# Kernel tuning notes

Hardware: AMD Instinct MI355X
Metric: run time of the kernel (lower is better)

Reference implementation:

```python
import jax, jax.numpy as jnp
import numpy as np

N, LQ, C = 1, 12240, 256
HEADS, LEVELS, FRAMES, POINTS = 8, 4, 4, 4
D_HEAD = C // HEADS  # 32
SHAPES = np.array([[48, 48, 4], [24, 24, 4], [12, 12, 4], [6, 6, 4]], np.int32)  # (H, W, T)
LEN_IN = int((SHAPES[:, 0] * SHAPES[:, 1] * SHAPES[:, 2]).sum())  # 12240
assert LEN_IN == LQ


def setup_inputs() -> dict:
    key = jax.random.key(0)
    ks = jax.random.split(key, 9)
    starts = np.concatenate([[0], np.cumsum(SHAPES[:, 0] * SHAPES[:, 1] * SHAPES[:, 2])[:-1]]).astype(np.int32)
    off_dim = HEADS * LEVELS * FRAMES * POINTS * 2
    attn_dim = HEADS * LEVELS * FRAMES * POINTS
    s = 1.0 / np.sqrt(C)
    return {
        "query": jax.random.normal(ks[0], (N, LQ, C), jnp.float32),
        "reference_points": jax.random.uniform(ks[1], (N, LQ, LEVELS, 2), dtype=jnp.float32),
        "temporal_offsets": 0.05 * jax.random.normal(ks[2], (LQ, LEVELS, FRAMES, 2), jnp.float32),
        "input_flatten": jax.random.normal(ks[3], (N, LEN_IN, C), jnp.float32),
        "input_spatial_shapes": jnp.asarray(SHAPES),
        "input_level_start_index": jnp.asarray(starts),
        "W_off": 0.01 * jax.random.normal(ks[4], (C, off_dim), jnp.float32),
        "b_off": 0.1 * jax.random.normal(ks[5], (off_dim,), jnp.float32),
        "W_attn": 0.02 * jax.random.normal(ks[6], (C, attn_dim), jnp.float32),
        "b_attn": jnp.zeros((attn_dim,), jnp.float32),
        "W_val": s * jax.random.normal(ks[7], (C, C), jnp.float32),
        "b_val": jnp.zeros((C,), jnp.float32),
        "W_out": s * jax.random.normal(ks[8], (C, C), jnp.float32),
        "b_out": jnp.zeros((C,), jnp.float32),
    }


def ms_deform_core(value, shapes_hw, starts, loc, attn_w):
    """value: (N, Len_in, Hh, D); loc: (N, Lq, Hh, L, P, 2) in [0,1];
    attn_w: (N, Lq, Hh, L, P); shapes_hw/starts: python ints per level.
    Bilinear sampling matches F.grid_sample(align_corners=False, padding_mode='zeros')."""
    n, _, hh, d = value.shape
    lq, p = loc.shape[1], loc.shape[4]
    out = jnp.zeros((n, hh, lq, d), value.dtype)
    for lid, (hl, wl) in enumerate(shapes_hw):
        s0 = starts[lid]
        v = jnp.transpose(value[:, s0:s0 + hl * wl], (0, 2, 1, 3))  # (N, Hh, H*W, D)
        x = loc[:, :, :, lid, :, 0] * wl - 0.5  # (N, Lq, Hh, P) pixel coords
        y = loc[:, :, :, lid, :, 1] * hl - 0.5
        x0 = jnp.floor(x)
        y0 = jnp.floor(y)
        fx, fy = x - x0, y - y0
        x0i, y0i = x0.astype(jnp.int32), y0.astype(jnp.int32)
        acc = jnp.zeros((n, hh, lq, p, d), value.dtype)
        corners = ((0, 0, (1 - fx) * (1 - fy)), (0, 1, fx * (1 - fy)),
                   (1, 0, (1 - fx) * fy), (1, 1, fx * fy))
        for dy, dx, w in corners:
            xi, yi = x0i + dx, y0i + dy
            valid = (xi >= 0) & (xi < wl) & (yi >= 0) & (yi < hl)
            idx = jnp.clip(yi, 0, hl - 1) * wl + jnp.clip(xi, 0, wl - 1)  # (N, Lq, Hh, P)
            idx_t = jnp.transpose(idx, (0, 2, 1, 3)).reshape(n, hh, lq * p, 1)
            g = jnp.take_along_axis(v, idx_t, axis=2).reshape(n, hh, lq, p, d)
            wm = jnp.transpose(jnp.where(valid, w, 0.0), (0, 2, 1, 3))  # (N, Hh, Lq, P)
            acc = acc + g * wm[..., None]
        aw = jnp.transpose(attn_w[:, :, :, lid], (0, 2, 1, 3))  # (N, Hh, Lq, P)
        out = out + jnp.sum(acc * aw[..., None], axis=3)
    return jnp.transpose(out, (0, 2, 1, 3)).reshape(n, lq, hh * d)


def reference(query, reference_points, temporal_offsets, input_flatten,
              input_spatial_shapes, input_level_start_index,
              W_off, b_off, W_attn, b_attn, W_val, b_val, W_out, b_out):
    shapes = np.asarray(input_spatial_shapes)  # static (L, 3) = (H, W, T)
    starts = [int(s) for s in np.asarray(input_level_start_index)]
    n, lq, _ = query.shape
    value = (input_flatten @ W_val + b_val).reshape(n, -1, HEADS, D_HEAD)
    attn = jax.nn.softmax((query @ W_attn + b_attn)
                          .reshape(n, lq, HEADS, LEVELS * FRAMES * POINTS), axis=-1)
    attn = attn.reshape(n, lq, HEADS, LEVELS, FRAMES * POINTS)
    off = (query @ W_off + b_off).reshape(n, lq, HEADS, LEVELS, FRAMES, POINTS, 2)
    # offset_normalizer = (T, H*W) per level: x spans frames, y spans flattened pixels
    norm = jnp.stack([jnp.asarray(shapes[:, 2], jnp.float32),
                      jnp.asarray(shapes[:, 0] * shapes[:, 1], jnp.float32)], axis=-1)  # (L, 2)
    loc = temporal_offsets[None, :, None, :, :, None, :] + off / norm[None, None, None, :, None, None, :]
    loc = loc.reshape(n, lq, HEADS, LEVELS, FRAMES * POINTS, 2)
    loc = reference_points[:, :, None, :, None, :] + loc
    shapes_hw = [(int(h) * int(w), int(t)) for h, w, t in shapes]  # (H*W, T) grids
    out = ms_deform_core(value, shapes_hw, starts, loc, attn)
    return out @ W_out + b_out
```

## Files before the change

### kernel.cpp

```cpp
#include <hip/hip_runtime.h>
#include <hip/hip_bf16.h>
#include <hip/hip_fp16.h>

#define LQ     12240

typedef _Float16 half8 __attribute__((ext_vector_type(8)));
typedef float floatx4 __attribute__((ext_vector_type(4)));
typedef unsigned int uint;

__global__ __launch_bounds__(256) void prep_all(
    const float* __restrict__ query, const float* __restrict__ inflat,
    const float* __restrict__ W_val, const float* __restrict__ W_attn,
    const float* __restrict__ W_off, const float* __restrict__ W_out,
    __half* __restrict__ qh, __half* __restrict__ ifh,
    __half* __restrict__ wT_val, __half* __restrict__ wT_ao,
    __half* __restrict__ wT_out, int n4each) {
  int b = blockIdx.x;
  if (b < 512) {
    const float* in;
    __half* out;
    int N;
    if (b < 64) { in = W_val; out = wT_val; N = 256; }
    else if (b < 192) { b -= 64; in = W_attn; out = wT_ao; N = 512; }
    else if (b < 448) { b -= 192; in = W_off; out = wT_ao + (size_t)512 * 256; N = 1024; }
    else { b -= 448; in = W_out; out = wT_out; N = 256; }
    const int nb = N / 32;
    const int n0 = (b % nb) * 32, k0 = (b / nb) * 32;

    __shared__ float t[32][33];
    const int c = threadIdx.x & 31, r = threadIdx.x >> 5;
#pragma unroll
    for (int i = 0; i < 4; ++i)
      t[r + i * 8][c] = in[(size_t)(k0 + r + i * 8) * N + n0 + c];
    __syncthreads();
#pragma unroll
    for (int i = 0; i < 4; ++i)
      out[(size_t)(n0 + r + i * 8) * 256 + k0 + c] = __float2half(t[c][r + i * 8]);
    return;
  }
  int i = (b - 512) * 256 + threadIdx.x;
  const float* in = query;
  __half* out = qh;
  if (i >= n4each) { in = inflat; out = ifh; i -= n4each; }
  const float4 v = reinterpret_cast<const float4*>(in)[i];
  const __half2 p0 = __floats2half2_rn(v.x, v.y);
  const __half2 p1 = __floats2half2_rn(v.z, v.w);
  uint2 pk;
  pk.x = *reinterpret_cast<const uint*>(&p0);
  pk.y = *reinterpret_cast<const uint*>(&p1);
  reinterpret_cast<uint2*>(out)[i] = pk;
}

__global__ __launch_bounds__(256) void gemm_all(
    const __half* __restrict__ qh, const __half* __restrict__ ifh,
    const __half* __restrict__ wT_val, const __half* __restrict__ wT_ao,
    const float* __restrict__ b_val, const float* __restrict__ b_attn,
    const float* __restrict__ b_off,
    __half* __restrict__ val_t, __half* __restrict__ ao_h, int M) {
  __shared__ uint4 As_g[128 * 8];
  __shared__ uint4 Bs_g[128 * 8];

  const int tid = threadIdx.x;

  const int nwg = gridDim.x * gridDim.y;
  int bid = blockIdx.y * gridDim.x + blockIdx.x;
  bid = (bid & 7) * (nwg >> 3) + (bid >> 3);
  const int bx = bid % gridDim.x;
  const int bm = (bid / gridDim.x) * 128;

  const bool isval = (bx < 2);
  const int bn = isval ? bx * 128 : (bx - 2) * 128;
  const __half* __restrict__ A  = isval ? ifh : qh;
  const __half* __restrict__ Bt = isval ? wT_val : wT_ao;
  const float* __restrict__ bias = isval ? b_val : (bn < 512 ? b_attn : b_off);
  const int coff = (!isval && bn >= 512) ? 512 : 0;

  const int wid = tid >> 6, lane = tid & 63;
  const int wr = wid >> 1, wn = wid & 1;
  const int l16 = lane & 15, lhi = lane >> 4;

  floatx4 acc[4][4] = {};

  const int srow = tid >> 1;
  const int sg0 = (tid & 1) * 4;
  const bool arow_ok = (bm + srow) < M;
  const __half* Arow = A + (size_t)(arow_ok ? bm + srow : 0) * 256;
  const __half* Brow = Bt + (size_t)(bn + srow) * 256;

  for (int ks = 0; ks < 4; ++ks) {
    const int k0 = ks * 64;
#pragma unroll
    for (int i = 0; i < 4; ++i) {
      const int g = sg0 + i;
      uint4 av = make_uint4(0, 0, 0, 0);
      if (arow_ok) av = *reinterpret_cast<const uint4*>(Arow + k0 + g * 8);
      As_g[srow * 8 + (g ^ (srow & 7))] = av;
      Bs_g[srow * 8 + (g ^ (srow & 7))] =
          *reinterpret_cast<const uint4*>(Brow + k0 + g * 8);
    }
    __syncthreads();

#pragma unroll
    for (int kk = 0; kk < 2; ++kk) {
      half8 a[4], b[4];
#pragma unroll
      for (int m = 0; m < 4; ++m) {
        const int row = wr * 64 + m * 16 + l16;
        const int g = kk * 4 + lhi;
        union { uint4 u; half8 h; } cv;
        cv.u = As_g[row * 8 + (g ^ (row & 7))];
        a[m] = cv.h;
      }
#pragma unroll
      for (int n = 0; n < 4; ++n) {
        const int row = wn * 64 + n * 16 + l16;
        const int g = kk * 4 + lhi;
        union { uint4 u; half8 h; } cv;
        cv.u = Bs_g[row * 8 + (g ^ (row & 7))];
        b[n] = cv.h;
      }
#pragma unroll
      for (int m = 0; m < 4; ++m)
#pragma unroll
        for (int n = 0; n < 4; ++n)
          acc[m][n] = __builtin_amdgcn_mfma_f32_16x16x32_f16(a[m], b[n], acc[m][n], 0, 0, 0);
    }
    __syncthreads();
  }

#pragma unroll
  for (int m = 0; m < 4; ++m) {
    const int row0 = bm + wr * 64 + m * 16 + lhi * 4;
#pragma unroll
    for (int n = 0; n < 4; ++n) {
      const int col = bn + wn * 64 + n * 16 + l16;
      const float bv = bias[col - coff];
#pragma unroll
      for (int r = 0; r < 4; ++r) {
        const int row = row0 + r;
        if (row < M) {
          const float v = acc[m][n][r] + bv;
          if (isval) {
            val_t[(size_t)(col >> 5) * ((size_t)M * 32) + (size_t)row * 32 + (col & 31)] = __float2half(v);
          } else {
            ao_h[(size_t)row * 1536 + col] = __float2half(v);
          }
        }
      }
    }
  }
}

__global__ __launch_bounds__(256) void gemm_out(
    const __half* __restrict__ A, const __half* __restrict__ Bt,
    const float* __restrict__ bias, float* __restrict__ C, int M, int N) {
  __shared__ uint4 As_g[128 * 8];
  __shared__ uint4 Bs_g[128 * 8];

  const int tid = threadIdx.x;
  const int nwg = gridDim.x * gridDim.y;
  int bid = blockIdx.y * gridDim.x + blockIdx.x;
  bid = (bid & 7) * (nwg >> 3) + (bid >> 3);
  const int bm = (bid / gridDim.x) * 128, bn = (bid % gridDim.x) * 128;

  const int wid = tid >> 6, lane = tid & 63;
  const int wr = wid >> 1, wn = wid & 1;
  const int l16 = lane & 15, lhi = lane >> 4;

  floatx4 acc[4][4] = {};

  const int srow = tid >> 1;
  const int sg0 = (tid & 1) * 4;
  const bool arow_ok = (bm + srow) < M;
  const __half* Arow = A + (size_t)(arow_ok ? bm + srow : 0) * 256;
  const __half* Brow = Bt + (size_t)(bn + srow) * 256;

  for (int ks = 0; ks < 4; ++ks) {
    const int k0 = ks * 64;
#pragma unroll
    for (int i = 0; i < 4; ++i) {
      const int g = sg0 + i;
      uint4 av = make_uint4(0, 0, 0, 0);
      if (arow_ok) av = *reinterpret_cast<const uint4*>(Arow + k0 + g * 8);
      As_g[srow * 8 + (g ^ (srow & 7))] = av;
      Bs_g[srow * 8 + (g ^ (srow & 7))] =
          *reinterpret_cast<const uint4*>(Brow + k0 + g * 8);
    }
    __syncthreads();

#pragma unroll
    for (int kk = 0; kk < 2; ++kk) {
      half8 a[4], b[4];
#pragma unroll
      for (int m = 0; m < 4; ++m) {
        const int row = wr * 64 + m * 16 + l16;
        const int g = kk * 4 + lhi;
        union { uint4 u; half8 h; } cv;
        cv.u = As_g[row * 8 + (g ^ (row & 7))];
        a[m] = cv.h;
      }
#pragma unroll
      for (int n = 0; n < 4; ++n) {
        const int row = wn * 64 + n * 16 + l16;
        const int g = kk * 4 + lhi;
        union { uint4 u; half8 h; } cv;
        cv.u = Bs_g[row * 8 + (g ^ (row & 7))];
        b[n] = cv.h;
      }
#pragma unroll
      for (int m = 0; m < 4; ++m)
#pragma unroll
        for (int n = 0; n < 4; ++n)
          acc[m][n] = __builtin_amdgcn_mfma_f32_16x16x32_f16(a[m], b[n], acc[m][n], 0, 0, 0);
    }
    __syncthreads();
  }

#pragma unroll
  for (int m = 0; m < 4; ++m) {
    const int row0 = bm + wr * 64 + m * 16 + lhi * 4;
#pragma unroll
    for (int n = 0; n < 4; ++n) {
      const int col = bn + wn * 64 + n * 16 + l16;
      const float bv = bias[col];
#pragma unroll
      for (int r = 0; r < 4; ++r) {
        const int row = row0 + r;
        if (row < M) C[(size_t)row * N + col] = acc[m][n][r] + bv;
      }
    }
  }
}

__device__ inline uint pack_wr(float w, uint row) {
  const __half hw = __float2half(w);
  return ((uint)__half_as_ushort(hw) << 16) | row;
}

__global__ __launch_bounds__(256, 8) void sample_kernel(
    const __half* __restrict__ value,
    const __half* __restrict__ ao,
    const float* __restrict__ tempoff,
    const float* __restrict__ refpts,
    __half* __restrict__ msout) {
  const int q0 = blockIdx.x * 2;
  const int tid = threadIdx.x;

  __shared__ __align__(16) uint spk[4096];
  float* slog = reinterpret_cast<float*>(spk);
  __shared__ float sm_m[16], sm_si[16];

#pragma unroll
  for (int k = 0; k < 4; ++k) {
    const int s = tid + k * 256;
    slog[s] = __half2float(ao[(size_t)(q0 + (s >> 9)) * 1536 + (s & 511)]);
  }
  __syncthreads();

  {
    const int g = tid >> 4;
    const int j = tid & 15;
    const float* e = &slog[g * 64];
    float m = fmaxf(fmaxf(e[j], e[j + 16]), fmaxf(e[j + 32], e[j + 48]));
#pragma unroll
    for (int mask = 8; mask >= 1; mask >>= 1) m = fmaxf(m, __shfl_xor(m, mask));
    float s = __expf(e[j] - m) + __expf(e[j + 16] - m) +
              __expf(e[j + 32] - m) + __expf(e[j + 48] - m);
#pragma unroll
    for (int mask = 8; mask >= 1; mask >>= 1) s += __shfl_xor(s, mask);
    if (j == 0) { sm_m[g] = m; sm_si[g] = 1.0f / s; }
  }
  __syncthreads();

  const float HWF[4] = {2304.f, 576.f, 144.f, 36.f};
  const float RHW[4] = {1.f / 2304.f, 1.f / 576.f, 1.f / 144.f, 1.f / 36.f};
  const int   S0[4]  = {0, 9216, 11520, 12096};
  const int   HWI[4] = {2304, 576, 144, 36};

  uint4 rec[4];
  int   ridx[4];
  const int h1   = tid & 7;
  const int smid = (tid >> 3) & 7;
  const int shi  = (tid >> 6) & 3;

#pragma unroll
  for (int k = 0; k < 4; ++k) {
    const int qi = k & 1;
    const int s  = smid | (shi << 3) | ((k >> 1) << 5);
    const int i  = h1 * 64 + s;
    const int l  = s >> 4;
    const int f  = (s >> 2) & 3;
    const size_t q = (size_t)(q0 + qi);
    const int g = (qi << 3) | h1;

    const float w = __expf(slog[(qi << 9) + i] - sm_m[g]) * sm_si[g];

    const float2 o  = __half22float2(*reinterpret_cast<const __half2*>(&ao[q * 1536 + 512 + i * 2]));
    const float2 to = *reinterpret_cast<const float2*>(&tempoff[q * 32 + (l * 4 + f) * 2]);
    const float2 rp = *reinterpret_cast<const float2*>(&refpts[q * 8 + l * 2]);

    const float hw = HWF[l];
    const float x = (to.x + o.x * 0.25f + rp.x) * 4.0f - 0.5f;
    const float y = (to.y + o.y * RHW[l] + rp.y) * hw - 0.5f;

    const float x0f = floorf(x), y0f = floorf(y);
    const float fx = x - x0f, fy = y - y0f;
    const int x0 = (int)x0f, y0 = (int)y0f;
    const int hl = HWI[l];

    const bool xv0 = (x0 >= 0) && (x0 < 4);
    const bool xv1 = (x0 >= -1) && (x0 < 3);
    const bool yv0 = (y0 >= 0) && (y0 < hl);
    const bool yv1 = (y0 >= -1) && (y0 < hl - 1);
    const int xc0 = min(max(x0, 0), 3);
    const int xc1 = min(max(x0 + 1, 0), 3);
    const int yc0 = min(max(y0, 0), hl - 1);
    const int yc1 = min(max(y0 + 1, 0), hl - 1);

    const float w00 = (xv0 && yv0) ? w * (1.f - fx) * (1.f - fy) : 0.f;
    const float w01 = (xv1 && yv0) ? w * fx * (1.f - fy) : 0.f;
    const float w10 = (xv0 && yv1) ? w * (1.f - fx) * fy : 0.f;
    const float w11 = (xv1 && yv1) ? w * fx * fy : 0.f;

    const int base = S0[l];
    rec[k] = make_uint4(pack_wr(w00, (uint)(base + yc0 * 4 + xc0)),
                        pack_wr(w01, (uint)(base + yc0 * 4 + xc1)),
                        pack_wr(w10, (uint)(base + yc1 * 4 + xc0)),
                        pack_wr(w11, (uint)(base + yc1 * 4 + xc1)));
    ridx[k] = (qi << 9) | (s << 3) | h1;
  }
  __syncthreads();

  uint4* spk4 = reinterpret_cast<uint4*>(spk);
#pragma unroll
  for (int k = 0; k < 4; ++k) spk4[ridx[k]] = rec[k];
  __syncthreads();

  const int qi = tid >> 7;
  const int h  = (tid >> 4) & 7;
  const int c  = (tid >> 2) & 3;
  const int d  = tid & 3;

  const uint* __restrict__ sp = spk + ((qi << 11) | (h << 2) | c);
  const char* __restrict__ vbase =
      (const char*)value + (size_t)h * LQ * 64 + d * 16;

  float f0 = 0.f, f1 = 0.f, f2 = 0.f, f3 = 0.f;
  float f4 = 0.f, f5 = 0.f, f6 = 0.f, f7 = 0.f;

#pragma unroll
  for (int l = 0; l < 4; ++l) {
    uint a0 = 0u, a1 = 0u, a2 = 0u, a3 = 0u;
#pragma unroll
    for (int t = 0; t < 16; ++t) {
      const uint pk = sp[(l * 16 + t) << 5];
      const uint4 v = *reinterpret_cast<const uint4*>(vbase + ((pk & 0xFFFFu) << 6));
      asm("v_pk_fma_f16 %0, %4, %5, %0 op_sel:[1,0,0]\n\t"
          "v_pk_fma_f16 %1, %4, %6, %1 op_sel:[1,0,0]\n\t"
          "v_pk_fma_f16 %2, %4, %7, %2 op_sel:[1,0,0]\n\t"
          "v_pk_fma_f16 %3, %4, %8, %3 op_sel:[1,0,0]"
          : "+v"(a0), "+v"(a1), "+v"(a2), "+v"(a3)
          : "v"(pk), "v"(v.x), "v"(v.y), "v"(v.z), "v"(v.w));
    }
    const float2 p0 = __half22float2(*reinterpret_cast<const __half2*>(&a0));
    const float2 p1 = __half22float2(*reinterpret_cast<const __half2*>(&a1));
    const float2 p2 = __half22float2(*reinterpret_cast<const __half2*>(&a2));
    const float2 p3 = __half22float2(*reinterpret_cast<const __half2*>(&a3));
    f0 += p0.x; f1 += p0.y; f2 += p1.x; f3 += p1.y;
    f4 += p2.x; f5 += p2.y; f6 += p3.x; f7 += p3.y;
  }

#pragma unroll
  for (int mask = 4; mask <= 8; mask <<= 1) {
    f0 += __shfl_xor(f0, mask); f1 += __shfl_xor(f1, mask);
    f2 += __shfl_xor(f2, mask); f3 += __shfl_xor(f3, mask);
    f4 += __shfl_xor(f4, mask); f5 += __shfl_xor(f5, mask);
    f6 += __shfl_xor(f6, mask); f7 += __shfl_xor(f7, mask);
  }

  if (c == 0) {
    const __half2 o0 = __floats2half2_rn(f0, f1);
    const __half2 o1 = __floats2half2_rn(f2, f3);
    const __half2 o2 = __floats2half2_rn(f4, f5);
    const __half2 o3 = __floats2half2_rn(f6, f7);
    uint4 st;
    st.x = *reinterpret_cast<const uint*>(&o0);
    st.y = *reinterpret_cast<const uint*>(&o1);
    st.z = *reinterpret_cast<const uint*>(&o2);
    st.w = *reinterpret_cast<const uint*>(&o3);
    *reinterpret_cast<uint4*>(&msout[(size_t)(q0 + qi) * 256 + h * 32 + d * 8]) = st;
  }
}

extern "C" void kernel_launch(void* const* d_in, const int* in_sizes, int n_in,
                              void* d_out, int out_size, void* d_ws, size_t ws_size,
                              hipStream_t stream) {
  const float* query   = (const float*)d_in[0];
  const float* refpts  = (const float*)d_in[1];
  const float* tempoff = (const float*)d_in[2];
  const float* inflat  = (const float*)d_in[3];
  const float* W_off  = (const float*)d_in[6];
  const float* b_off  = (const float*)d_in[7];
  const float* W_attn = (const float*)d_in[8];
  const float* b_attn = (const float*)d_in[9];
  const float* W_val  = (const float*)d_in[10];
  const float* b_val  = (const float*)d_in[11];
  const float* W_out  = (const float*)d_in[12];
  const float* b_out  = (const float*)d_in[13];

  char* ws = (char*)d_ws;
  const size_t szQ = (size_t)LQ * 256 * 2;
  __half* qh     = (__half*)ws;                 ws += szQ;
  __half* ifh    = (__half*)ws;                 ws += szQ;
  __half* wT_val = (__half*)ws;                 ws += (size_t)256 * 256 * 2;
  __half* wT_ao  = (__half*)ws;                 ws += (size_t)1536 * 256 * 2;
  __half* wT_out = (__half*)ws;                 ws += (size_t)256 * 256 * 2;
  __half* val_t  = (__half*)ws;                 ws += szQ;
  __half* ao_h   = (__half*)ws;                 ws += (size_t)LQ * 1536 * 2;
  __half* ms_h   = (__half*)ws;                 ws += szQ;

  const dim3 blk(256);
  const int n4each = LQ * 256 / 4;

  prep_all<<<dim3(512 + 2 * n4each / 256), blk, 0, stream>>>(
      query, inflat, W_val, W_attn, W_off, W_out,
      qh, ifh, wT_val, wT_ao, wT_out, n4each);

  const int gm = (LQ + 127) / 128;
  gemm_all<<<dim3(14, gm), blk, 0, stream>>>(qh, ifh, wT_val, wT_ao,
                                             b_val, b_attn, b_off,
                                             val_t, ao_h, LQ);

  sample_kernel<<<dim3(LQ / 2), blk, 0, stream>>>(val_t, ao_h, tempoff, refpts, ms_h);

  gemm_out<<<dim3(2, gm), blk, 0, stream>>>(ms_h, wT_out, b_out, (float*)d_out, LQ, 256);
}
```

Before: 124.8 us.

## Merge horizontally adjacent bilinear corners into one contiguous 128-byte gather per row

The bilinear corner records are restructured so each sample row (y0, y1) stores one base index plus a packed pair of half weights for the two adjacent x-corners. When the x-corners are not adjacent, for example after clamping at a border, both weights fold into the low slot. Threads now split 8 ways over a 128-byte span covering two neighbouring value rows, and pick the matching weight with a byte permute. This halves the number of shared-memory record reads and gather instructions per sample. In exchange it relies on the two x-corners being contiguous rows in the value layout and changes the reduction lane mapping.

```diff
diff --git a/kernel.cpp b/kernel.cpp
--- a/kernel.cpp
+++ b/kernel.cpp
@@ -232,9 +232,9 @@
   }
 }
 
-__device__ inline uint pack_wr(float w, uint row) {
-  const __half hw = __float2half(w);
-  return ((uint)__half_as_ushort(hw) << 16) | row;
+__device__ inline uint pack2h(float lo, float hi) {
+  const __half2 p = __floats2half2_rn(lo, hi);
+  return *reinterpret_cast<const uint*>(&p);
 }
 
 __global__ __launch_bounds__(256, 8) void sample_kernel(
@@ -317,16 +317,17 @@
     const int yc0 = min(max(y0, 0), hl - 1);
     const int yc1 = min(max(y0 + 1, 0), hl - 1);
 
-    const float w00 = (xv0 && yv0) ? w * (1.f - fx) * (1.f - fy) : 0.f;
-    const float w01 = (xv1 && yv0) ? w * fx * (1.f - fy) : 0.f;
-    const float w10 = (xv0 && yv1) ? w * (1.f - fx) * fy : 0.f;
-    const float w11 = (xv1 && yv1) ? w * fx * fy : 0.f;
+    const bool adj = (xc1 == xc0 + 1);
+    const float fxlo = (xv0 ? (1.f - fx) : 0.f) + ((!adj && xv1) ? fx : 0.f);
+    const float fxhi = (adj && xv1) ? fx : 0.f;
+    const float wy0 = yv0 ? w * (1.f - fy) : 0.f;
+    const float wy1 = yv1 ? w * fy : 0.f;
 
     const int base = S0[l];
-    rec[k] = make_uint4(pack_wr(w00, (uint)(base + yc0 * 4 + xc0)),
-                        pack_wr(w01, (uint)(base + yc0 * 4 + xc1)),
-                        pack_wr(w10, (uint)(base + yc1 * 4 + xc0)),
-                        pack_wr(w11, (uint)(base + yc1 * 4 + xc1)));
+    rec[k] = make_uint4((uint)(base + yc0 * 4 + xc0),
+                        pack2h(fxlo * wy0, fxhi * wy0),
+                        (uint)(base + yc1 * 4 + xc0),
+                        pack2h(fxlo * wy1, fxhi * wy1));
     ridx[k] = (qi << 9) | (s << 3) | h1;
   }
   __syncthreads();
@@ -338,12 +339,14 @@
 
   const int qi = tid >> 7;
   const int h  = (tid >> 4) & 7;
-  const int c  = (tid >> 2) & 3;
-  const int d  = tid & 3;
-
-  const uint* __restrict__ sp = spk + ((qi << 11) | (h << 2) | c);
+  const int yc = (tid >> 3) & 1;
+  const int d  = tid & 7;
+
+  const uint2* __restrict__ sp2 =
+      reinterpret_cast<const uint2*>(spk) + ((qi << 10) | (h << 1) | yc);
   const char* __restrict__ vbase =
       (const char*)value + (size_t)h * LQ * 64 + d * 16;
+  const uint sel = (d < 4) ? 0x01000100u : 0x03020302u;
 
   float f0 = 0.f, f1 = 0.f, f2 = 0.f, f3 = 0.f;
   float f4 = 0.f, f5 = 0.f, f6 = 0.f, f7 = 0.f;
@@ -353,14 +356,15 @@
     uint a0 = 0u, a1 = 0u, a2 = 0u, a3 = 0u;
 #pragma unroll
     for (int t = 0; t < 16; ++t) {
-      const uint pk = sp[(l * 16 + t) << 5];
-      const uint4 v = *reinterpret_cast<const uint4*>(vbase + ((pk & 0xFFFFu) << 6));
-      asm("v_pk_fma_f16 %0, %4, %5, %0 op_sel:[1,0,0]\n\t"
-          "v_pk_fma_f16 %1, %4, %6, %1 op_sel:[1,0,0]\n\t"
-          "v_pk_fma_f16 %2, %4, %7, %2 op_sel:[1,0,0]\n\t"
-          "v_pk_fma_f16 %3, %4, %8, %3 op_sel:[1,0,0]"
+      const uint2 rc = sp2[(l * 16 + t) << 4];
+      const uint wdup = __builtin_amdgcn_perm(rc.y, rc.y, sel);
+      const uint4 v = *reinterpret_cast<const uint4*>(vbase + ((size_t)rc.x << 6));
+      asm("v_pk_fma_f16 %0, %4, %5, %0\n\t"
+          "v_pk_fma_f16 %1, %4, %6, %1\n\t"
+          "v_pk_fma_f16 %2, %4, %7, %2\n\t"
+          "v_pk_fma_f16 %3, %4, %8, %3"
           : "+v"(a0), "+v"(a1), "+v"(a2), "+v"(a3)
-          : "v"(pk), "v"(v.x), "v"(v.y), "v"(v.z), "v"(v.w));
+          : "v"(wdup), "v"(v.x), "v"(v.y), "v"(v.z), "v"(v.w));
     }
     const float2 p0 = __half22float2(*reinterpret_cast<const __half2*>(&a0));
     const float2 p1 = __half22float2(*reinterpret_cast<const __half2*>(&a1));
@@ -378,7 +382,7 @@
     f6 += __shfl_xor(f6, mask); f7 += __shfl_xor(f7, mask);
   }
 
-  if (c == 0) {
+  if ((tid & 12) == 0) {
     const __half2 o0 = __floats2half2_rn(f0, f1);
     const __half2 o1 = __floats2half2_rn(f2, f3);
     const __half2 o2 = __floats2half2_rn(f4, f5);
@@ -388,7 +392,7 @@
     st.y = *reinterpret_cast<const uint*>(&o1);
     st.z = *reinterpret_cast<const uint*>(&o2);
     st.w = *reinterpret_cast<const uint*>(&o3);
-    *reinterpret_cast<uint4*>(&msout[(size_t)(q0 + qi) * 256 + h * 32 + d * 8]) = st;
+    *reinterpret_cast<uint4*>(&msout[(size_t)(q0 + qi) * 256 + h * 32 + (tid & 3) * 8]) = st;
   }
 }
 
```

Measured after the change: 126.0 us. No clear change (+1.0%).
